# Kernel optimization log

Measured on AMD Instinct MI355X. Metric: run time of the kernel, lower is better.

Reference implementation:

```python
import jax, jax.numpy as jnp
import numpy as np
from jax import lax

# program token ids
PAD, START, END, SCENE, INTERSECT, FILT, RELATE, QUERY = range(8)
SKIP = (PAD, START, END)


def conv2d(x, w, b, dil=1):
    # 'same' padding for odd kernels (3x3 pad=dil, 1x1 pad=0), NCHW/OIHW
    pad = dil * (w.shape[2] // 2)
    y = lax.conv_general_dilated(x, w, (1, 1), [(pad, pad), (pad, pad)],
                                 rhs_dilation=(dil, dil),
                                 dimension_numbers=('NCHW', 'OIHW', 'NCHW'))
    return y + b[None, :, None, None]


def maxpool2(x):
    return lax.reduce_window(x, -jnp.inf, lax.max, (1, 1, 2, 2), (1, 1, 2, 2), 'VALID')


def exec_program(prog, feat_input, p):
    """Run one (concrete) program over a batch of stem features. prog: tuple of ints,
    executed in reversed order exactly like TbDNet.forward."""
    B, _, H, W = feat_input.shape
    output = feat_input
    saved = None
    for t in reversed(prog):
        if t in SKIP:
            continue
        if t == SCENE:
            saved = output
            output = jnp.ones((B, 1, H, W), feat_input.dtype)
        elif t == INTERSECT:  # AndModule: elementwise min of attentions
            output = jnp.minimum(output, saved)
        elif t == FILT:
            a = feat_input * output  # [B,D,H,W] * [B,1,H,W]
            a = jax.nn.relu(conv2d(a, p['att_w1'], p['att_b1']))
            a = jax.nn.relu(conv2d(a, p['att_w2'], p['att_b2']))
            output = jax.nn.sigmoid(conv2d(a, p['att_w3'], p['att_b3']))
        elif t == RELATE:  # RelateModule: dilated conv stack (1,2,4,8,1) -> conv1x1 sigmoid
            a = feat_input * output
            for w, b, d in ((p['rel_w1'], p['rel_b1'], 1), (p['rel_w2'], p['rel_b2'], 2),
                            (p['rel_w3'], p['rel_b3'], 4), (p['rel_w4'], p['rel_b4'], 8),
                            (p['rel_w5'], p['rel_b5'], 1)):
                a = jax.nn.relu(conv2d(a, w, b, d))
            output = jax.nn.sigmoid(conv2d(a, p['rel_w6'], p['rel_b6']))
        elif t == QUERY:
            a = feat_input * output
            a = jax.nn.relu(conv2d(a, p['qry_w1'], p['qry_b1']))
            output = jax.nn.relu(conv2d(a, p['qry_w2'], p['qry_b2']))
    return output


def tbd_forward(feats, programs_np, p):
    B = feats.shape[0]
    stem = jax.nn.relu(conv2d(feats, p['stem_w1'], p['stem_b1']))
    stem = jax.nn.relu(conv2d(stem, p['stem_w2'], p['stem_b2']))  # [B,D,H,W]
    D, H, W = stem.shape[1], stem.shape[2], stem.shape[3]
    # group samples by identical program so dispatch runs batched, not per-sample
    groups = {}
    for n in range(B):
        groups.setdefault(tuple(int(v) for v in programs_np[n]), []).append(n)
    mod_out = jnp.zeros((B, D, H, W), feats.dtype)
    for prog, idxs in groups.items():
        idx = jnp.array(idxs)
        mod_out = mod_out.at[idx].set(exec_program(prog, stem[idx], p))
    # classifier: conv1x1 -> relu -> maxpool2 -> flatten -> fc -> relu -> fc
    x = jax.nn.relu(conv2d(mod_out, p['cls_w'], p['cls_b']))
    x = maxpool2(x)                        # [B,1024,7,7]
    x = x.reshape(B, -1)                   # [B,50176]
    x = jax.nn.relu(x @ p['fc1_w'].T + p['fc1_b'])
    return x @ p['fc2_w'].T + p['fc2_b']   # [B,28]


def setup_inputs() -> dict:
    key = jax.random.key(0)
    ks = iter(jax.random.split(key, 64))
    def rn(shape, s=0.05):
        return jax.random.normal(next(ks), shape, dtype=jnp.float32) * s
    B, Cin, H, W, D, P, L, A = 64, 1024, 14, 14, 128, 1024, 1024, 28
    feats = jax.random.normal(next(ks), (B, Cin, H, W), dtype=jnp.float32)
    # stored programs; execution order is reversed(stored)
    progA = [START, QUERY, FILT, RELATE, FILT, SCENE, END, PAD]            # scene->filter->relate->filter->query
    progB = [START, QUERY, INTERSECT, FILT, SCENE, FILT, SCENE, END]       # two filter branches -> intersect -> query
    programs = jnp.array([progA] * (B // 2) + [progB] * (B // 2), dtype=jnp.int32)
    inp = {'feats': feats, 'programs': programs,
           'stem_w1': rn((D, Cin, 3, 3), 0.02), 'stem_b1': rn((D,)),
           'stem_w2': rn((D, D, 3, 3)), 'stem_b2': rn((D,)),
           'att_w1': rn((D, D, 3, 3)), 'att_b1': rn((D,)),
           'att_w2': rn((D, D, 3, 3)), 'att_b2': rn((D,)),
           'att_w3': rn((1, D, 1, 1)), 'att_b3': rn((1,)),
           'rel_w1': rn((D, D, 3, 3)), 'rel_b1': rn((D,)),
           'rel_w2': rn((D, D, 3, 3)), 'rel_b2': rn((D,)),
           'rel_w3': rn((D, D, 3, 3)), 'rel_b3': rn((D,)),
           'rel_w4': rn((D, D, 3, 3)), 'rel_b4': rn((D,)),
           'rel_w5': rn((D, D, 3, 3)), 'rel_b5': rn((D,)),
           'rel_w6': rn((1, D, 1, 1)), 'rel_b6': rn((1,)),
           'qry_w1': rn((D, D, 3, 3)), 'qry_b1': rn((D,)),
           'qry_w2': rn((D, D, 3, 3)), 'qry_b2': rn((D,)),
           'cls_w': rn((P, D, 1, 1)), 'cls_b': rn((P,)),
           'fc1_w': rn((L, P * (H // 2) * (W // 2)), 0.01), 'fc1_b': rn((L,)),
           'fc2_w': rn((A, L)), 'fc2_b': rn((A,))}
    return inp


PARAM_NAMES = ['stem_w1', 'stem_b1', 'stem_w2', 'stem_b2',
               'att_w1', 'att_b1', 'att_w2', 'att_b2', 'att_w3', 'att_b3',
               'rel_w1', 'rel_b1', 'rel_w2', 'rel_b2', 'rel_w3', 'rel_b3',
               'rel_w4', 'rel_b4', 'rel_w5', 'rel_b5', 'rel_w6', 'rel_b6',
               'qry_w1', 'qry_b1', 'qry_w2', 'qry_b2',
               'cls_w', 'cls_b', 'fc1_w', 'fc1_b', 'fc2_w', 'fc2_b']


def reference(feats, programs, stem_w1, stem_b1, stem_w2, stem_b2,
              att_w1, att_b1, att_w2, att_b2, att_w3, att_b3,
              rel_w1, rel_b1, rel_w2, rel_b2, rel_w3, rel_b3,
              rel_w4, rel_b4, rel_w5, rel_b5, rel_w6, rel_b6,
              qry_w1, qry_b1, qry_w2, qry_b2,
              cls_w, cls_b, fc1_w, fc1_b, fc2_w, fc2_b):
    vals = [stem_w1, stem_b1, stem_w2, stem_b2,
            att_w1, att_b1, att_w2, att_b2, att_w3, att_b3,
            rel_w1, rel_b1, rel_w2, rel_b2, rel_w3, rel_b3,
            rel_w4, rel_b4, rel_w5, rel_b5, rel_w6, rel_b6,
            qry_w1, qry_b1, qry_w2, qry_b2,
            cls_w, cls_b, fc1_w, fc1_b, fc2_w, fc2_b]
    p = dict(zip(PARAM_NAMES, vals))
    return tbd_forward(feats, np.asarray(programs), p)
```

## Files before the change

kernel.cpp:

```cpp
#include <hip/hip_runtime.h>
#include <math.h>


typedef __attribute__((ext_vector_type(8)))  short   short8;
typedef __attribute__((ext_vector_type(8)))  __bf16  bf16x8;
typedef __attribute__((ext_vector_type(4)))  float   f32x4;

#define NROUNDS 15
#define NKS 49

#define B_WSTEM1 0UL
#define B_WSTEM2 2359296UL
#define B_WMOD   2654208UL
#define B_WCLS   5308416UL
#define B_STEM   5570560UL
#define B_XA     8781824UL
#define B_XB     11993088UL
#define B_FEAT   15204352UL
#define B_ATTN   18415616UL
#define B_SAVED  18465792UL
#define B_SCHED  18515968UL
#define B_ACTB   18520064UL
#define B_FC1T   24942592UL
#define B_S1P    B_XB
#define B_FC1P   B_STEM

__device__ __forceinline__ unsigned short f2bf(float f) {
    unsigned int b = __float_as_uint(f);
    b += 0x7fffu + ((b >> 16) & 1u);
    return (unsigned short)(b >> 16);
}
__device__ __forceinline__ float bf2f(unsigned short u) {
    return __uint_as_float(((unsigned int)u) << 16);
}
__device__ __forceinline__ f32x4 mfma16(bf16x8 a, bf16x8 b, f32x4 c) {
    return __builtin_amdgcn_mfma_f32_16x16x32_bf16(a, b, c, 0, 0, 0);
}

struct RepackArgs { const float* src[12]; };

__global__ __launch_bounds__(256) void k_repack(RepackArgs a, char* ws)
{
    const int y = blockIdx.y;
    const float* __restrict__ src = a.src[y];
    int gid = blockIdx.x * 256 + threadIdx.x;
    int gsz = gridDim.x * 256;
    if (y == 11) {
        unsigned short* dst = (unsigned short*)(ws + B_WCLS);
        for (int i = gid; i < 131072; i += gsz) dst[i] = f2bf(src[i]);
    } else {
        const int IC = (y == 0) ? 1024 : 128;
        const int lg = (y == 0) ? 10 : 7;
        unsigned short* dst = (unsigned short*)(ws + ((y == 0) ? B_WSTEM1
                                    : (y == 1) ? B_WSTEM2
                                    : B_WMOD + (size_t)(y - 2) * 294912));
        const int total = 9 << (lg + 7);
        for (int i = gid; i < total; i += gsz) {
            int ic = i & (IC - 1);
            int oc = (i >> lg) & 127;
            int t  = i >> (lg + 7);
            dst[i] = f2bf(src[((size_t)oc * IC + ic) * 9 + t]);
        }
    }
}

__global__ __launch_bounds__(256) void k_decode_init(const int* __restrict__ prog, char* ws)
{
    int gid = blockIdx.x * 256 + threadIdx.x;
    int gsz = gridDim.x * 256;
    float* attn  = (float*)(ws + B_ATTN);
    float* saved = (float*)(ws + B_SAVED);
    for (int i = gid; i < 64 * 196; i += gsz) { attn[i] = 1.0f; saved[i] = 1.0f; }
    unsigned int* fz = (unsigned int*)(ws + B_FEAT);
    for (int i = gid; i < 64 * 25088 / 2; i += gsz) fz[i] = 0u;
    if (gid < 64) {
        int n = gid;
        int ent[NROUNDS];
        for (int r = 0; r < NROUNDS; ++r) ent[r] = 0;
        int rc = 0;
#define ENC(op,wv,dl,g,s,d) ((op)|((wv)<<4)|((dl)<<8)|((g)<<12)|((s)<<13)|((d)<<15))
#define EMIT(v) do { if (rc < NROUNDS) ent[rc++] = (v); } while (0)
        for (int j = 7; j >= 0; --j) {
            int t = prog[n * 8 + j];
            switch (t) {
                case 3: EMIT(ENC(1,0,0,0,0,0)); break;
                case 4: EMIT(ENC(2,0,0,0,0,0)); break;
                case 5:
                    EMIT(ENC(3,0,1,1,3,0));
                    EMIT(ENC(3,1,1,0,0,1));
                    EMIT(ENC(4,0,0,0,1,0));
                    break;
                case 6:
                    EMIT(ENC(3,2,1,1,3,0));
                    EMIT(ENC(3,3,2,0,0,1));
                    EMIT(ENC(3,4,4,0,1,0));
                    EMIT(ENC(3,5,8,0,0,1));
                    EMIT(ENC(3,6,1,0,1,0));
                    EMIT(ENC(4,1,0,0,0,0));
                    break;
                case 7:
                    EMIT(ENC(3,7,1,1,3,0));
                    EMIT(ENC(3,8,1,0,0,2));
                    break;
                default: break;
            }
        }
#undef EMIT
#undef ENC
        int* sched = (int*)(ws + B_SCHED);
        for (int r = 0; r < NROUNDS; ++r) sched[n * NROUNDS + r] = ent[r];
    }
}

__global__ __launch_bounds__(512) void k_stem1p(const float* __restrict__ feats,
                                                const unsigned short* __restrict__ wrep,
                                                char* ws)
{
    __shared__ unsigned short s_img[197 * 136];
    const int bx = blockIdx.x;
    const int n = bx >> 2, ks = bx & 3;
    const int tid = threadIdx.x, lane = tid & 63;
    const int w = tid >> 6, wm = w & 1, wn = w >> 1;
    const int l15 = lane & 15, lq = lane >> 4;

    if (tid < 68) ((unsigned int*)s_img)[196 * 68 + tid] = 0u;

    int pglob[4], pbyt[4], pyv[4], pxv[4];
#pragma unroll
    for (int j = 0; j < 4; ++j) {
        int p  = (wn + 4 * j) * 16 + l15;
        pglob[j] = p;
        int py = p / 14;
        pyv[j] = (p < 196) ? py : 10000;
        pxv[j] = p - py * 14;
        pbyt[j] = p * 272 + lq * 16;
    }
    const int zaddr = 196 * 272 + lq * 16;
    const int nJ = (wn == 0) ? 4 : 3;

    f32x4 acc[4][4];
#pragma unroll
    for (int m = 0; m < 4; ++m)
#pragma unroll
        for (int j = 0; j < 4; ++j) acc[m][j] = (f32x4){0.f, 0.f, 0.f, 0.f};

    const int icg = tid & 31;
    const int qq0 = tid >> 5;

    for (int slab = 0; slab < 2; ++slab) {
        if (slab) __syncthreads();
        const int icb = ks * 256 + slab * 128;
        const float* sf = feats + ((size_t)n * 1024 + icb) * 196;
        for (int qq = qq0; qq < 49; qq += 16) {
            const float* p0 = sf + icg * 4 * 196 + qq * 4;
            float4 r0 = *(const float4*)(p0);
            float4 r1 = *(const float4*)(p0 + 196);
            float4 r2 = *(const float4*)(p0 + 392);
            float4 r3 = *(const float4*)(p0 + 588);
#pragma unroll
            for (int e = 0; e < 4; ++e) {
                uint2 v;
                v.x = (unsigned int)f2bf(((const float*)&r0)[e]) |
                      ((unsigned int)f2bf(((const float*)&r1)[e]) << 16);
                v.y = (unsigned int)f2bf(((const float*)&r2)[e]) |
                      ((unsigned int)f2bf(((const float*)&r3)[e]) << 16);
                *(uint2*)(s_img + (qq * 4 + e) * 136 + icg * 4) = v;
            }
        }
        __syncthreads();

#pragma unroll
        for (int t = 0; t < 9; ++t) {
            const int dy = t / 3 - 1, dx = t % 3 - 1;
            int baddr[4];
#pragma unroll
            for (int j = 0; j < 4; ++j) {
                int yy = pyv[j] + dy, xx = pxv[j] + dx;
                bool ok = ((unsigned)yy < 14u) && ((unsigned)xx < 14u);
                baddr[j] = ok ? (pbyt[j] + (dy * 14 + dx) * 272) : zaddr;
            }
#pragma unroll
            for (int kc = 0; kc < 4; ++kc) {
                const unsigned short* wt = wrep +
                    ((size_t)(t * 128 + wm * 64 + l15) * 1024 + icb + kc * 32 + lq * 8);
                bf16x8 am[4];
#pragma unroll
                for (int m = 0; m < 4; ++m)
                    am[m] = *(const bf16x8*)(wt + (size_t)m * 16 * 1024);
#pragma unroll
                for (int j = 0; j < 4; ++j) {
                    if (j < nJ) {
                        bf16x8 b = *(const bf16x8*)((const char*)s_img + baddr[j] + kc * 64);
#pragma unroll
                        for (int m = 0; m < 4; ++m)
                            acc[m][j] = mfma16(am[m], b, acc[m][j]);
                    }
                }
            }
        }
    }

    unsigned short* part = (unsigned short*)(ws + B_S1P);
#pragma unroll
    for (int m = 0; m < 4; ++m) {
        const int oc = wm * 64 + m * 16 + lq * 4;
#pragma unroll
        for (int j = 0; j < 4; ++j) {
            if (j < nJ) {
                int p = pglob[j];
                if (p < 196) {
                    unsigned int lo = (unsigned int)f2bf(acc[m][j][0]) |
                                      ((unsigned int)f2bf(acc[m][j][1]) << 16);
                    unsigned int hi = (unsigned int)f2bf(acc[m][j][2]) |
                                      ((unsigned int)f2bf(acc[m][j][3]) << 16);
                    uint2 pk; pk.x = lo; pk.y = hi;
                    *(uint2*)(part + (((size_t)ks * 64 + n) * 196 + p) * 128 + oc) = pk;
                }
            }
        }
    }
}

__global__ __launch_bounds__(256) void k_stem1r(const char* __restrict__ ws_c,
                                                const float* __restrict__ bias,
                                                unsigned short* __restrict__ xa)
{
    int i = blockIdx.x * 256 + threadIdx.x;
    const unsigned short* part = (const unsigned short*)(ws_c + B_S1P);
    int oc8 = (i & 15) * 8;
    int np  = i >> 4;
    float s[8] = {};
#pragma unroll
    for (int ks = 0; ks < 4; ++ks) {
        short8 v = *(const short8*)(part + (((size_t)ks * 64) * 196 + np) * 128 + oc8);
#pragma unroll
        for (int e = 0; e < 8; ++e) s[e] += bf2f((unsigned short)v[e]);
    }
    short8 o;
#pragma unroll
    for (int e = 0; e < 8; ++e)
        o[e] = (short)f2bf(fmaxf(s[e] + bias[oc8 + e], 0.f));
    *(short8*)(xa + (size_t)np * 128 + oc8) = o;
}

__device__ void conv_mfma_core(const unsigned short* __restrict__ srcB,
                               const float*  __restrict__ gate,
                               const unsigned short* __restrict__ wrep,
                               const float*  __restrict__ bias,
                               unsigned short* __restrict__ dst,
                               int dil, int oct, int pxh,
                               unsigned short* s_img)
{
    const int tid  = threadIdx.x, lane = tid & 63;
    const int w    = tid >> 6, wm = w & 1, wn = w >> 1;
    const int l15  = lane & 15, lq = lane >> 4;

    if (tid < 68) ((unsigned int*)s_img)[196 * 68 + tid] = 0u;

    int pglob[4], pbyt[4], pyv[4], pxv[4];
#pragma unroll
    for (int j = 0; j < 4; ++j) {
        int nt = wn + 2 * j;
        int p  = (pxh * 7 + nt) * 16 + l15;
        pglob[j] = p;
        int py = p / 14;
        pyv[j] = (p < 196) ? py : 10000;
        pxv[j] = p - py * 14;
        pbyt[j] = p * 272 + lq * 16;
    }
    const int zaddr = 196 * 272 + lq * 16;
    const int nNT = (wn == 0) ? 4 : 3;

    f32x4 acc[4];
#pragma unroll
    for (int j = 0; j < 4; ++j) acc[j] = (f32x4){0.f, 0.f, 0.f, 0.f};

    if (gate) {
        for (int i = tid; i < 196 * 16; i += 256) {
            int p = i >> 4, c8 = (i & 15) * 8;
            short8 v = *(const short8*)(srcB + p * 128 + c8);
            float g = gate[p];
            short8 ov;
#pragma unroll
            for (int e = 0; e < 8; ++e)
                ov[e] = (short)f2bf(bf2f((unsigned short)v[e]) * g);
            *(short8*)(s_img + p * 136 + c8) = ov;
        }
    } else {
        for (int i = tid; i < 196 * 16; i += 256) {
            int p = i >> 4, c8 = (i & 15) * 8;
            *(short8*)(s_img + p * 136 + c8) = *(const short8*)(srcB + p * 128 + c8);
        }
    }
    __syncthreads();

    const unsigned short* wlane = wrep + (size_t)(oct * 32 + wm * 16 + l15) * 128 + lq * 8;
#pragma unroll
    for (int t = 0; t < 9; ++t) {
        const int dy = (t / 3 - 1) * dil, dx = (t % 3 - 1) * dil;
        int baddr[4];
#pragma unroll
        for (int j = 0; j < 4; ++j) {
            int yy = pyv[j] + dy, xx = pxv[j] + dx;
            bool ok = ((unsigned)yy < 14u) && ((unsigned)xx < 14u);
            baddr[j] = ok ? (pbyt[j] + (dy * 14 + dx) * 272) : zaddr;
        }
        const unsigned short* wt = wlane + (size_t)(t * 128) * 128;
#pragma unroll
        for (int kc = 0; kc < 4; ++kc) {
            bf16x8 a0 = *(const bf16x8*)(wt + kc * 32);
#pragma unroll
            for (int j = 0; j < 4; ++j) {
                if (j < nNT) {
                    bf16x8 b = *(const bf16x8*)((const char*)s_img + baddr[j] + kc * 64);
                    acc[j] = mfma16(a0, b, acc[j]);
                }
            }
        }
    }

    const int oc = oct * 32 + wm * 16 + lq * 4;
    const float4 b4 = *(const float4*)(bias + oc);
#pragma unroll
    for (int j = 0; j < 4; ++j) {
        if (j < nNT) {
            int p = pglob[j];
            if (p < 196) {
                float v0 = fmaxf(acc[j][0] + b4.x, 0.f);
                float v1 = fmaxf(acc[j][1] + b4.y, 0.f);
                float v2 = fmaxf(acc[j][2] + b4.z, 0.f);
                float v3 = fmaxf(acc[j][3] + b4.w, 0.f);
                uint2 pk;
                pk.x = (unsigned int)f2bf(v0) | ((unsigned int)f2bf(v1) << 16);
                pk.y = (unsigned int)f2bf(v2) | ((unsigned int)f2bf(v3) << 16);
                *(uint2*)(dst + p * 128 + oc) = pk;
            }
        }
    }
}

__global__ __launch_bounds__(256) void k_conv_stem2(const unsigned short* __restrict__ srcBall,
                                                    const unsigned short* __restrict__ wrep,
                                                    const float* __restrict__ bias,
                                                    unsigned short* __restrict__ dstall)
{
    __shared__ unsigned short s_img[197 * 136];
    const int n = blockIdx.x >> 3, oct = (blockIdx.x >> 1) & 3, pxh = blockIdx.x & 1;
    conv_mfma_core(srcBall + (size_t)n * 25088, nullptr, wrep, bias,
                   dstall + (size_t)n * 25088, 1, oct, pxh, s_img);
}

struct RArgs {
    char* ws;
    const float* mbias[9];
    const float* w1x1[2];
    const float* b1x1[2];
};

__global__ __launch_bounds__(256) void k_round(RArgs a, int r)
{
    __shared__ unsigned short s_img[197 * 136];
    const int bx = blockIdx.x;
    const int n = bx >> 3, oct = (bx >> 1) & 3, pxh = bx & 1;
    char* ws = a.ws;
    const int* sched = (const int*)(ws + B_SCHED);
    const int e = sched[n * NROUNDS + r];
    const int op = e & 15;
    if (op == 0) return;
    float* attn  = (float*)(ws + B_ATTN)  + n * 196;
    float* saved = (float*)(ws + B_SAVED) + n * 196;
    if (op == 1 || op == 2) {
        if ((bx & 7) == 0 && threadIdx.x < 196) {
            int p = threadIdx.x;
            if (op == 1) { saved[p] = attn[p]; attn[p] = 1.0f; }
            else         attn[p] = fminf(attn[p], saved[p]);
        }
        return;
    }
    const int wset = (e >> 4) & 15, dil = (e >> 8) & 15, gatef = (e >> 12) & 1;
    const int srcid = (e >> 13) & 3, dstid = (e >> 15) & 3;
    const unsigned short* src = (const unsigned short*)(ws +
            (srcid == 3 ? B_STEM : srcid == 1 ? B_XB : B_XA)) + (size_t)n * 25088;
    if (op == 4) {
        if ((bx & 7) == 0 && threadIdx.x < 196) {
            int p = threadIdx.x;
            const float* wv = a.w1x1[wset];
            float acc = a.b1x1[wset][0];
            const unsigned short* row = src + p * 128;
#pragma unroll 8
            for (int ic = 0; ic < 128; ++ic) acc += bf2f(row[ic]) * wv[ic];
            attn[p] = 1.0f / (1.0f + __expf(-acc));
        }
        return;
    }
    unsigned short* dst = (unsigned short*)(ws +
            (dstid == 2 ? B_FEAT : dstid == 1 ? B_XB : B_XA)) + (size_t)n * 25088;
    const unsigned short* wrep = (const unsigned short*)(ws + B_WMOD) + (size_t)wset * 9 * 128 * 128;
    conv_mfma_core(src, gatef ? attn : nullptr, wrep, a.mbias[wset], dst,
                   dil, oct, pxh, s_img);
}

__global__ __launch_bounds__(256) void k_cls_pool(const unsigned short* __restrict__ featall,
                                                  const unsigned short* __restrict__ clsw,
                                                  const float* __restrict__ clsb,
                                                  unsigned short* __restrict__ actB)
{
    __shared__ char smem[197 * 272 + 64 * 200 * 4];
    unsigned short* s_img = (unsigned short*)smem;
    float* s_pool = (float*)(smem + 197 * 272);
    const int n = blockIdx.x >> 4, pt = blockIdx.x & 15;
    const int tid = threadIdx.x, lane = tid & 63, w = tid >> 6;
    const int l15 = lane & 15, lq = lane >> 4;
    const unsigned short* feat = featall + (size_t)n * 25088;

    if (tid < 68) ((unsigned int*)s_img)[196 * 68 + tid] = 0u;
    for (int i = tid; i < 196 * 16; i += 256) {
        int p = i >> 4, c8 = (i & 15) * 8;
        *(short8*)(s_img + p * 136 + c8) = *(const short8*)(feat + p * 128 + c8);
    }
    f32x4 acc[14];
#pragma unroll
    for (int j = 0; j < 14; ++j) acc[j] = (f32x4){0.f, 0.f, 0.f, 0.f};
    __syncthreads();

    const unsigned short* wl = clsw + (size_t)(pt * 64 + w * 16 + l15) * 128 + lq * 8;
#pragma unroll
    for (int kc = 0; kc < 4; ++kc) {
        bf16x8 a0 = *(const bf16x8*)(wl + kc * 32);
#pragma unroll
        for (int j = 0; j < 14; ++j) {
            int p = j * 16 + l15;
            int ba = (p < 196) ? (p * 272 + lq * 16 + kc * 64) : (196 * 272 + lq * 16);
            bf16x8 b = *(const bf16x8*)((const char*)s_img + ba);
            acc[j] = mfma16(a0, b, acc[j]);
        }
    }
    const int oc = pt * 64 + w * 16 + lq * 4;
    const float4 b4 = *(const float4*)(clsb + oc);
    const int pl = w * 16 + lq * 4;
#pragma unroll
    for (int j = 0; j < 14; ++j) {
        int p = j * 16 + l15;
        if (p < 196) {
            s_pool[(pl + 0) * 200 + p] = fmaxf(acc[j][0] + b4.x, 0.f);
            s_pool[(pl + 1) * 200 + p] = fmaxf(acc[j][1] + b4.y, 0.f);
            s_pool[(pl + 2) * 200 + p] = fmaxf(acc[j][2] + b4.z, 0.f);
            s_pool[(pl + 3) * 200 + p] = fmaxf(acc[j][3] + b4.w, 0.f);
        }
    }
    __syncthreads();
    for (int i = tid; i < 64 * 49; i += 256) {
        int plx = i / 49, q = i - plx * 49;
        int py = q / 7, qx = q - py * 7;
        const float* rp = s_pool + plx * 200 + py * 28 + qx * 2;
        float m = fmaxf(fmaxf(rp[0], rp[1]), fmaxf(rp[14], rp[15]));
        int k = (pt * 64 + plx) * 49 + q;
        int kb = k >> 6, lq2 = (k >> 4) & 3, hi = (k >> 3) & 1, e = k & 7;
        actB[((((size_t)kb * 4 + lq2) * 2 + hi) * 64 + n) * 8 + e] = f2bf(m);
    }
}

__global__ __launch_bounds__(256) void k_fc1p(const unsigned short* __restrict__ actB,
                                              const float* __restrict__ w,
                                              float* __restrict__ part)
{
    __shared__ unsigned short s_w[64 * 264];
    const int jt = blockIdx.x & 15, ks = blockIdx.x >> 4;
    const int tid = threadIdx.x, lane = tid & 63, wv = tid >> 6;
    const int l15 = lane & 15, lq = lane >> 4;
    const int k0 = ks * 1024;
    const int r4 = tid & 3, l4 = (tid >> 2) & 15, rw = tid >> 6;

    f32x4 acc[4];
#pragma unroll
    for (int t = 0; t < 4; ++t) acc[t] = (f32x4){0.f, 0.f, 0.f, 0.f};

    float4 pf[4][4];

#define FC1_LOAD(ss_) do {                                                        \
    _Pragma("unroll")                                                             \
    for (int pass = 0; pass < 4; ++pass) {                                        \
        const int row_ = pass * 16 + rw * 4 + r4;                                 \
        const float* wp_ = w + (size_t)(jt * 64 + row_) * 50176 + k0              \
                             + (ss_) * 256 + l4 * 16;                             \
        pf[pass][0] = *(const float4*)(wp_);                                      \
        pf[pass][1] = *(const float4*)(wp_ + 4);                                  \
        pf[pass][2] = *(const float4*)(wp_ + 8);                                  \
        pf[pass][3] = *(const float4*)(wp_ + 12);                                 \
    } } while (0)

    FC1_LOAD(0);

    for (int ss = 0; ss < 4; ++ss) {
        __syncthreads();
#pragma unroll
        for (int pass = 0; pass < 4; ++pass) {
            const int row = pass * 16 + rw * 4 + r4;
            bf16x8 c0, c1;
            c0[0] = (__bf16)pf[pass][0].x; c0[1] = (__bf16)pf[pass][0].y;
            c0[2] = (__bf16)pf[pass][0].z; c0[3] = (__bf16)pf[pass][0].w;
            c0[4] = (__bf16)pf[pass][1].x; c0[5] = (__bf16)pf[pass][1].y;
            c0[6] = (__bf16)pf[pass][1].z; c0[7] = (__bf16)pf[pass][1].w;
            c1[0] = (__bf16)pf[pass][2].x; c1[1] = (__bf16)pf[pass][2].y;
            c1[2] = (__bf16)pf[pass][2].z; c1[3] = (__bf16)pf[pass][2].w;
            c1[4] = (__bf16)pf[pass][3].x; c1[5] = (__bf16)pf[pass][3].y;
            c1[6] = (__bf16)pf[pass][3].z; c1[7] = (__bf16)pf[pass][3].w;
            *(bf16x8*)(s_w + row * 264 + l4 * 16)     = c0;
            *(bf16x8*)(s_w + row * 264 + l4 * 16 + 8) = c1;
        }
        __syncthreads();
        if (ss < 3) FC1_LOAD(ss + 1);

        const unsigned short* arow = s_w + (wv * 16 + l15) * 264;
#pragma unroll
        for (int kk = 0; kk < 8; ++kk) {
            bf16x8 a = *(const bf16x8*)(arow + kk * 32 + lq * 8);
            const int kglob = k0 + ss * 256 + kk * 32 + lq * 8;
            const int kb = kglob >> 6, lq2 = (kglob >> 4) & 3, hi = (kglob >> 3) & 1;
            const unsigned short* bp = actB +
                ((((size_t)kb * 4 + lq2) * 2 + hi) * 64 + l15) * 8;
#pragma unroll
            for (int t = 0; t < 4; ++t) {
                bf16x8 b = *(const bf16x8*)(bp + t * 128);
                acc[t] = mfma16(a, b, acc[t]);
            }
        }
    }
#undef FC1_LOAD

    float* pbase = part + ((size_t)ks * 1024 + jt * 64 + wv * 16 + lq * 4) * 64 + l15;
#pragma unroll
    for (int t = 0; t < 4; ++t)
#pragma unroll
        for (int r = 0; r < 4; ++r)
            pbase[(size_t)r * 64 + t * 16] = acc[t][r];
}

__global__ __launch_bounds__(256) void k_fc1r(const float* __restrict__ part,
                                              const float* __restrict__ b,
                                              float* __restrict__ fc1T)
{
    int i = blockIdx.x * 256 + threadIdx.x;
    if (i >= 65536) return;
    float s = 0.0f;
    for (int ks = 0; ks < NKS; ++ks) s += part[(size_t)ks * 65536 + i];
    int j = i >> 6;
    fc1T[i] = fmaxf(s + b[j], 0.0f);
}

__global__ __launch_bounds__(256) void k_fc2(const float* __restrict__ fc1T,
                                             const float* __restrict__ w,
                                             const float* __restrict__ b,
                                             float* __restrict__ out)
{
    __shared__ float red[256];
    const int a_ = blockIdx.x;
    const int tid = threadIdx.x, lane = tid & 63, q = tid >> 6;
    float acc = 0.0f;
    const float* wr = w + (size_t)a_ * 1024;
    for (int k = q * 256; k < q * 256 + 256; ++k)
        acc = fmaf(fc1T[k * 64 + lane], wr[k], acc);
    red[tid] = acc;
    __syncthreads();
    if (q == 0) {
        float s = red[tid] + red[tid + 64] + red[tid + 128] + red[tid + 192] + b[a_];
        out[lane * 28 + a_] = s;
    }
}

extern "C" void kernel_launch(void* const* d_in, const int* in_sizes, int n_in,
                              void* d_out, int out_size, void* d_ws, size_t ws_size,
                              hipStream_t stream)
{
    const float* feats = (const float*)d_in[0];
    const int*   prog  = (const int*)d_in[1];
    char* ws  = (char*)d_ws;
    float* out = (float*)d_out;

    RepackArgs ra;
    ra.src[0]  = (const float*)d_in[2];
    ra.src[1]  = (const float*)d_in[4];
    ra.src[2]  = (const float*)d_in[6];
    ra.src[3]  = (const float*)d_in[8];
    ra.src[4]  = (const float*)d_in[12];
    ra.src[5]  = (const float*)d_in[14];
    ra.src[6]  = (const float*)d_in[16];
    ra.src[7]  = (const float*)d_in[18];
    ra.src[8]  = (const float*)d_in[20];
    ra.src[9]  = (const float*)d_in[24];
    ra.src[10] = (const float*)d_in[26];
    ra.src[11] = (const float*)d_in[28];

    k_repack<<<dim3(64, 12), 256, 0, stream>>>(ra, ws);

    k_stem1p<<<256, 512, 0, stream>>>(feats, (const unsigned short*)(ws + B_WSTEM1), ws);
    k_stem1r<<<784, 256, 0, stream>>>(ws, (const float*)d_in[3],
                                      (unsigned short*)(ws + B_XA));

    k_decode_init<<<256, 256, 0, stream>>>(prog, ws);

    k_conv_stem2<<<512, 256, 0, stream>>>((const unsigned short*)(ws + B_XA),
                                          (const unsigned short*)(ws + B_WSTEM2),
                                          (const float*)d_in[5],
                                          (unsigned short*)(ws + B_STEM));

    RArgs ga;
    ga.ws = ws;
    ga.mbias[0] = (const float*)d_in[7];
    ga.mbias[1] = (const float*)d_in[9];
    ga.mbias[2] = (const float*)d_in[13];
    ga.mbias[3] = (const float*)d_in[15];
    ga.mbias[4] = (const float*)d_in[17];
    ga.mbias[5] = (const float*)d_in[19];
    ga.mbias[6] = (const float*)d_in[21];
    ga.mbias[7] = (const float*)d_in[25];
    ga.mbias[8] = (const float*)d_in[27];
    ga.w1x1[0]  = (const float*)d_in[10];
    ga.w1x1[1]  = (const float*)d_in[22];
    ga.b1x1[0]  = (const float*)d_in[11];
    ga.b1x1[1]  = (const float*)d_in[23];

    for (int r = 0; r < NROUNDS; ++r)
        k_round<<<512, 256, 0, stream>>>(ga, r);

    k_cls_pool<<<1024, 256, 0, stream>>>((const unsigned short*)(ws + B_FEAT),
                                         (const unsigned short*)(ws + B_WCLS),
                                         (const float*)d_in[29],
                                         (unsigned short*)(ws + B_ACTB));
    k_fc1p<<<784, 256, 0, stream>>>((const unsigned short*)(ws + B_ACTB),
                                    (const float*)d_in[30], (float*)(ws + B_FC1P));
    k_fc1r<<<256, 256, 0, stream>>>((const float*)(ws + B_FC1P), (const float*)d_in[31],
                                    (float*)(ws + B_FC1T));
    k_fc2<<<28, 256, 0, stream>>>((const float*)(ws + B_FC1T), (const float*)d_in[32],
                                  (const float*)d_in[33], out);
}
```

Baseline: 546.1 us.

## Fuse scene/intersect/1x1 heads into conv rounds and split stem/fc1 reductions finer

Removes the separate scene, intersect and 1x1-sigmoid rounds by folding them into the conv epilogue and the next conv's gate prologue. The 1x1 projection is now accumulated with atomics into per-slot buffers, and the sigmoid plus scene/intersect bookkeeping is applied when the next gated conv starts. This cuts the round count from 15 to 12 launches. Separately, the stem1 and fc1 K-splits are doubled to raise parallelism, which moves partial buffers to new workspace offsets and adds more partial-sum reduction work plus atomic contention.

```diff
diff --git a/kernel.cpp b/kernel.cpp
--- a/kernel.cpp
+++ b/kernel.cpp
@@ -6,8 +6,8 @@
 typedef __attribute__((ext_vector_type(8)))  __bf16  bf16x8;
 typedef __attribute__((ext_vector_type(4)))  float   f32x4;
 
-#define NROUNDS 15
-#define NKS 49
+#define NROUNDS 12
+#define NKS 98
 
 #define B_WSTEM1 0UL
 #define B_WSTEM2 2359296UL
@@ -22,8 +22,9 @@
 #define B_SCHED  18515968UL
 #define B_ACTB   18520064UL
 #define B_FC1T   24942592UL
-#define B_S1P    B_XB
-#define B_FC1P   B_STEM
+#define B_P1X1   25204736UL
+#define B_S1P    67108864UL
+#define B_FC1P   100663296UL
 
 __device__ __forceinline__ unsigned short f2bf(float f) {
     unsigned int b = __float_as_uint(f);
@@ -70,43 +71,57 @@
     int gsz = gridDim.x * 256;
     float* attn  = (float*)(ws + B_ATTN);
     float* saved = (float*)(ws + B_SAVED);
+    float* p1    = (float*)(ws + B_P1X1);
     for (int i = gid; i < 64 * 196; i += gsz) { attn[i] = 1.0f; saved[i] = 1.0f; }
+    for (int i = gid; i < 8 * 64 * 196; i += gsz) p1[i] = 0.0f;
     unsigned int* fz = (unsigned int*)(ws + B_FEAT);
     for (int i = gid; i < 64 * 25088 / 2; i += gsz) fz[i] = 0u;
     if (gid < 64) {
         int n = gid;
         int ent[NROUNDS];
         for (int r = 0; r < NROUNDS; ++r) ent[r] = 0;
-        int rc = 0;
-#define ENC(op,wv,dl,g,s,d) ((op)|((wv)<<4)|((dl)<<8)|((g)<<12)|((s)<<13)|((d)<<15))
+        int rc = 0, nslot = 0;
+        int pscene = 0, pinter = 0, pmat = 0, pmw = 0;
+#define PREBITS ((pscene<<17)|(pinter<<18)|(pmat<<19)|(pmw<<22))
+#define CLRPRE  (pscene = pinter = pmat = pmw = 0)
 #define EMIT(v) do { if (rc < NROUNDS) ent[rc++] = (v); } while (0)
         for (int j = 7; j >= 0; --j) {
             int t = prog[n * 8 + j];
             switch (t) {
-                case 3: EMIT(ENC(1,0,0,0,0,0)); break;
-                case 4: EMIT(ENC(2,0,0,0,0,0)); break;
-                case 5:
-                    EMIT(ENC(3,0,1,1,3,0));
-                    EMIT(ENC(3,1,1,0,0,1));
-                    EMIT(ENC(4,0,0,0,1,0));
+                case 3: pscene = 1; break;
+                case 4: pinter = 1; break;
+                case 5: {
+                    int e1 = 3 | (0<<4) | (1<<8) | (1<<12) | (2<<13) | (0<<15) | PREBITS;
+                    CLRPRE; EMIT(e1);
+                    int e2 = 3 | (1<<4) | (1<<8) | (0<<12) | (0<<13) | (1<<15)
+                               | (1<<23) | (0<<24) | (nslot<<25);
+                    EMIT(e2);
+                    pmat = nslot + 1; pmw = 0; nslot++;
                     break;
-                case 6:
-                    EMIT(ENC(3,2,1,1,3,0));
-                    EMIT(ENC(3,3,2,0,0,1));
-                    EMIT(ENC(3,4,4,0,1,0));
-                    EMIT(ENC(3,5,8,0,0,1));
-                    EMIT(ENC(3,6,1,0,1,0));
-                    EMIT(ENC(4,1,0,0,0,0));
+                }
+                case 6: {
+                    int e1 = 3 | (2<<4) | (1<<8) | (1<<12) | (2<<13) | (0<<15) | PREBITS;
+                    CLRPRE; EMIT(e1);
+                    EMIT(3 | (3<<4) | (2<<8) | (0<<12) | (0<<13) | (1<<15));
+                    EMIT(3 | (4<<4) | (4<<8) | (0<<12) | (1<<13) | (0<<15));
+                    EMIT(3 | (5<<4) | (8<<8) | (0<<12) | (0<<13) | (1<<15));
+                    EMIT(3 | (6<<4) | (1<<8) | (0<<12) | (1<<13) | (0<<15)
+                           | (1<<23) | (1<<24) | (nslot<<25));
+                    pmat = nslot + 1; pmw = 1; nslot++;
                     break;
-                case 7:
-                    EMIT(ENC(3,7,1,1,3,0));
-                    EMIT(ENC(3,8,1,0,0,2));
+                }
+                case 7: {
+                    int e1 = 3 | (7<<4) | (1<<8) | (1<<12) | (2<<13) | (0<<15) | PREBITS;
+                    CLRPRE; EMIT(e1);
+                    EMIT(3 | (8<<4) | (1<<8) | (0<<12) | (0<<13) | (2<<15));
                     break;
+                }
                 default: break;
             }
         }
 #undef EMIT
-#undef ENC
+#undef PREBITS
+#undef CLRPRE
         int* sched = (int*)(ws + B_SCHED);
         for (int r = 0; r < NROUNDS; ++r) sched[n * NROUNDS + r] = ent[r];
     }
@@ -118,7 +133,7 @@
 {
     __shared__ unsigned short s_img[197 * 136];
     const int bx = blockIdx.x;
-    const int n = bx >> 2, ks = bx & 3;
+    const int n = bx >> 3, ks = bx & 7;
     const int tid = threadIdx.x, lane = tid & 63;
     const int w = tid >> 6, wm = w & 1, wn = w >> 1;
     const int l15 = lane & 15, lq = lane >> 4;
@@ -146,55 +161,52 @@
 
     const int icg = tid & 31;
     const int qq0 = tid >> 5;
-
-    for (int slab = 0; slab < 2; ++slab) {
-        if (slab) __syncthreads();
-        const int icb = ks * 256 + slab * 128;
-        const float* sf = feats + ((size_t)n * 1024 + icb) * 196;
-        for (int qq = qq0; qq < 49; qq += 16) {
-            const float* p0 = sf + icg * 4 * 196 + qq * 4;
-            float4 r0 = *(const float4*)(p0);
-            float4 r1 = *(const float4*)(p0 + 196);
-            float4 r2 = *(const float4*)(p0 + 392);
-            float4 r3 = *(const float4*)(p0 + 588);
-#pragma unroll
-            for (int e = 0; e < 4; ++e) {
-                uint2 v;
-                v.x = (unsigned int)f2bf(((const float*)&r0)[e]) |
-                      ((unsigned int)f2bf(((const float*)&r1)[e]) << 16);
-                v.y = (unsigned int)f2bf(((const float*)&r2)[e]) |
-                      ((unsigned int)f2bf(((const float*)&r3)[e]) << 16);
-                *(uint2*)(s_img + (qq * 4 + e) * 136 + icg * 4) = v;
-            }
-        }
-        __syncthreads();
-
-#pragma unroll
-        for (int t = 0; t < 9; ++t) {
-            const int dy = t / 3 - 1, dx = t % 3 - 1;
-            int baddr[4];
+    const int icb = ks * 128;
+
+    const float* sf = feats + ((size_t)n * 1024 + icb) * 196;
+    for (int qq = qq0; qq < 49; qq += 16) {
+        const float* p0 = sf + icg * 4 * 196 + qq * 4;
+        float4 r0 = *(const float4*)(p0);
+        float4 r1 = *(const float4*)(p0 + 196);
+        float4 r2 = *(const float4*)(p0 + 392);
+        float4 r3 = *(const float4*)(p0 + 588);
+#pragma unroll
+        for (int e = 0; e < 4; ++e) {
+            uint2 v;
+            v.x = (unsigned int)f2bf(((const float*)&r0)[e]) |
+                  ((unsigned int)f2bf(((const float*)&r1)[e]) << 16);
+            v.y = (unsigned int)f2bf(((const float*)&r2)[e]) |
+                  ((unsigned int)f2bf(((const float*)&r3)[e]) << 16);
+            *(uint2*)(s_img + (qq * 4 + e) * 136 + icg * 4) = v;
+        }
+    }
+    __syncthreads();
+
+#pragma unroll
+    for (int t = 0; t < 9; ++t) {
+        const int dy = t / 3 - 1, dx = t % 3 - 1;
+        int baddr[4];
+#pragma unroll
+        for (int j = 0; j < 4; ++j) {
+            int yy = pyv[j] + dy, xx = pxv[j] + dx;
+            bool ok = ((unsigned)yy < 14u) && ((unsigned)xx < 14u);
+            baddr[j] = ok ? (pbyt[j] + (dy * 14 + dx) * 272) : zaddr;
+        }
+#pragma unroll
+        for (int kc = 0; kc < 4; ++kc) {
+            const unsigned short* wt = wrep +
+                ((size_t)(t * 128 + wm * 64 + l15) * 1024 + icb + kc * 32 + lq * 8);
+            bf16x8 am[4];
+#pragma unroll
+            for (int m = 0; m < 4; ++m)
+                am[m] = *(const bf16x8*)(wt + (size_t)m * 16 * 1024);
 #pragma unroll
             for (int j = 0; j < 4; ++j) {
-                int yy = pyv[j] + dy, xx = pxv[j] + dx;
-                bool ok = ((unsigned)yy < 14u) && ((unsigned)xx < 14u);
-                baddr[j] = ok ? (pbyt[j] + (dy * 14 + dx) * 272) : zaddr;
-            }
-#pragma unroll
-            for (int kc = 0; kc < 4; ++kc) {
-                const unsigned short* wt = wrep +
-                    ((size_t)(t * 128 + wm * 64 + l15) * 1024 + icb + kc * 32 + lq * 8);
-                bf16x8 am[4];
-#pragma unroll
-                for (int m = 0; m < 4; ++m)
-                    am[m] = *(const bf16x8*)(wt + (size_t)m * 16 * 1024);
-#pragma unroll
-                for (int j = 0; j < 4; ++j) {
-                    if (j < nJ) {
-                        bf16x8 b = *(const bf16x8*)((const char*)s_img + baddr[j] + kc * 64);
-#pragma unroll
-                        for (int m = 0; m < 4; ++m)
-                            acc[m][j] = mfma16(am[m], b, acc[m][j]);
-                    }
+                if (j < nJ) {
+                    bf16x8 b = *(const bf16x8*)((const char*)s_img + baddr[j] + kc * 64);
+#pragma unroll
+                    for (int m = 0; m < 4; ++m)
+                        acc[m][j] = mfma16(am[m], b, acc[m][j]);
                 }
             }
         }
@@ -231,7 +243,7 @@
     int np  = i >> 4;
     float s[8] = {};
 #pragma unroll
-    for (int ks = 0; ks < 4; ++ks) {
+    for (int ks = 0; ks < 8; ++ks) {
         short8 v = *(const short8*)(part + (((size_t)ks * 64) * 196 + np) * 128 + oc8);
 #pragma unroll
         for (int e = 0; e < 8; ++e) s[e] += bf2f((unsigned short)v[e]);
@@ -243,13 +255,15 @@
     *(short8*)(xa + (size_t)np * 128 + oc8) = o;
 }
 
-__device__ void conv_mfma_core(const unsigned short* __restrict__ srcB,
-                               const float*  __restrict__ gate,
-                               const unsigned short* __restrict__ wrep,
-                               const float*  __restrict__ bias,
-                               unsigned short* __restrict__ dst,
-                               int dil, int oct, int pxh,
-                               unsigned short* s_img)
+__device__ void conv_core32(const unsigned short* __restrict__ srcB,
+                            const float* __restrict__ s_gate,
+                            const unsigned short* __restrict__ wrep,
+                            const float* __restrict__ bias,
+                            unsigned short* __restrict__ dst,
+                            int dil, int oct, int pxh,
+                            unsigned short* s_img,
+                            int post, const float* __restrict__ pwv,
+                            float* __restrict__ pdst)
 {
     const int tid  = threadIdx.x, lane = tid & 63;
     const int w    = tid >> 6, wm = w & 1, wn = w >> 1;
@@ -275,11 +289,11 @@
 #pragma unroll
     for (int j = 0; j < 4; ++j) acc[j] = (f32x4){0.f, 0.f, 0.f, 0.f};
 
-    if (gate) {
+    if (s_gate) {
         for (int i = tid; i < 196 * 16; i += 256) {
             int p = i >> 4, c8 = (i & 15) * 8;
             short8 v = *(const short8*)(srcB + p * 128 + c8);
-            float g = gate[p];
+            float g = s_gate[p];
             short8 ov;
 #pragma unroll
             for (int e = 0; e < 8; ++e)
@@ -321,6 +335,8 @@
 
     const int oc = oct * 32 + wm * 16 + lq * 4;
     const float4 b4 = *(const float4*)(bias + oc);
+    float4 wv4;
+    if (post) wv4 = *(const float4*)(pwv + oc);
 #pragma unroll
     for (int j = 0; j < 4; ++j) {
         if (j < nNT) {
@@ -334,6 +350,10 @@
                 pk.x = (unsigned int)f2bf(v0) | ((unsigned int)f2bf(v1) << 16);
                 pk.y = (unsigned int)f2bf(v2) | ((unsigned int)f2bf(v3) << 16);
                 *(uint2*)(dst + p * 128 + oc) = pk;
+                if (post) {
+                    float s = v0 * wv4.x + v1 * wv4.y + v2 * wv4.z + v3 * wv4.w;
+                    atomicAdd(pdst + p, s);
+                }
             }
         }
     }
@@ -346,8 +366,8 @@
 {
     __shared__ unsigned short s_img[197 * 136];
     const int n = blockIdx.x >> 3, oct = (blockIdx.x >> 1) & 3, pxh = blockIdx.x & 1;
-    conv_mfma_core(srcBall + (size_t)n * 25088, nullptr, wrep, bias,
-                   dstall + (size_t)n * 25088, 1, oct, pxh, s_img);
+    conv_core32(srcBall + (size_t)n * 25088, nullptr, wrep, bias,
+                dstall + (size_t)n * 25088, 1, oct, pxh, s_img, 0, nullptr, nullptr);
 }
 
 struct RArgs {
@@ -360,44 +380,49 @@
 __global__ __launch_bounds__(256) void k_round(RArgs a, int r)
 {
     __shared__ unsigned short s_img[197 * 136];
+    __shared__ float s_gate[196];
     const int bx = blockIdx.x;
     const int n = bx >> 3, oct = (bx >> 1) & 3, pxh = bx & 1;
     char* ws = a.ws;
     const int* sched = (const int*)(ws + B_SCHED);
     const int e = sched[n * NROUNDS + r];
-    const int op = e & 15;
-    if (op == 0) return;
+    if ((e & 15) == 0) return;
+    const int tid = threadIdx.x;
+    const int wset = (e >> 4) & 15, dil = (e >> 8) & 15, gatef = (e >> 12) & 1;
+    const int srcid = (e >> 13) & 3, dstid = (e >> 15) & 3;
+    const int fscene = (e >> 17) & 1, finter = (e >> 18) & 1;
+    const int mslot = (e >> 19) & 7, mw = (e >> 22) & 1;
+    const int post = (e >> 23) & 1, pw = (e >> 24) & 1, pslot = (e >> 25) & 7;
+
     float* attn  = (float*)(ws + B_ATTN)  + n * 196;
     float* saved = (float*)(ws + B_SAVED) + n * 196;
-    if (op == 1 || op == 2) {
-        if ((bx & 7) == 0 && threadIdx.x < 196) {
-            int p = threadIdx.x;
-            if (op == 1) { saved[p] = attn[p]; attn[p] = 1.0f; }
-            else         attn[p] = fminf(attn[p], saved[p]);
-        }
-        return;
-    }
-    const int wset = (e >> 4) & 15, dil = (e >> 8) & 15, gatef = (e >> 12) & 1;
-    const int srcid = (e >> 13) & 3, dstid = (e >> 15) & 3;
+    float* p1    = (float*)(ws + B_P1X1);
+
+    if (gatef) {
+        if (tid < 196) {
+            float cur = attn[tid];
+            if (mslot) {
+                float pv = p1[(size_t)(mslot - 1) * 12544 + n * 196 + tid];
+                cur = 1.0f / (1.0f + __expf(-(pv + a.b1x1[mw][0])));
+            }
+            if (fscene) { saved[tid] = cur; cur = 1.0f; }
+            if (finter) { cur = fminf(cur, saved[tid]); }
+            if (mslot | fscene | finter) attn[tid] = cur;
+            s_gate[tid] = cur;
+        }
+        __syncthreads();
+    }
+
     const unsigned short* src = (const unsigned short*)(ws +
-            (srcid == 3 ? B_STEM : srcid == 1 ? B_XB : B_XA)) + (size_t)n * 25088;
-    if (op == 4) {
-        if ((bx & 7) == 0 && threadIdx.x < 196) {
-            int p = threadIdx.x;
-            const float* wv = a.w1x1[wset];
-            float acc = a.b1x1[wset][0];
-            const unsigned short* row = src + p * 128;
-#pragma unroll 8
-            for (int ic = 0; ic < 128; ++ic) acc += bf2f(row[ic]) * wv[ic];
-            attn[p] = 1.0f / (1.0f + __expf(-acc));
-        }
-        return;
-    }
+            (srcid == 2 ? B_STEM : srcid == 1 ? B_XB : B_XA)) + (size_t)n * 25088;
     unsigned short* dst = (unsigned short*)(ws +
             (dstid == 2 ? B_FEAT : dstid == 1 ? B_XB : B_XA)) + (size_t)n * 25088;
     const unsigned short* wrep = (const unsigned short*)(ws + B_WMOD) + (size_t)wset * 9 * 128 * 128;
-    conv_mfma_core(src, gatef ? attn : nullptr, wrep, a.mbias[wset], dst,
-                   dil, oct, pxh, s_img);
+
+    conv_core32(src, gatef ? s_gate : nullptr, wrep, a.mbias[wset], dst,
+                dil, oct, pxh, s_img,
+                post, post ? a.w1x1[pw] : nullptr,
+                post ? (p1 + (size_t)pslot * 12544 + n * 196) : nullptr);
 }
 
 __global__ __launch_bounds__(256) void k_cls_pool(const unsigned short* __restrict__ featall,
@@ -468,7 +493,7 @@
     const int jt = blockIdx.x & 15, ks = blockIdx.x >> 4;
     const int tid = threadIdx.x, lane = tid & 63, wv = tid >> 6;
     const int l15 = lane & 15, lq = lane >> 4;
-    const int k0 = ks * 1024;
+    const int k0 = ks * 512;
     const int r4 = tid & 3, l4 = (tid >> 2) & 15, rw = tid >> 6;
 
     f32x4 acc[4];
@@ -491,7 +516,7 @@
 
     FC1_LOAD(0);
 
-    for (int ss = 0; ss < 4; ++ss) {
+    for (int ss = 0; ss < 2; ++ss) {
         __syncthreads();
 #pragma unroll
         for (int pass = 0; pass < 4; ++pass) {
@@ -509,7 +534,7 @@
             *(bf16x8*)(s_w + row * 264 + l4 * 16 + 8) = c1;
         }
         __syncthreads();
-        if (ss < 3) FC1_LOAD(ss + 1);
+        if (ss < 1) FC1_LOAD(1);
 
         const unsigned short* arow = s_w + (wv * 16 + l15) * 264;
 #pragma unroll
@@ -592,12 +617,11 @@
     ra.src[11] = (const float*)d_in[28];
 
     k_repack<<<dim3(64, 12), 256, 0, stream>>>(ra, ws);
-
-    k_stem1p<<<256, 512, 0, stream>>>(feats, (const unsigned short*)(ws + B_WSTEM1), ws);
+    k_decode_init<<<256, 256, 0, stream>>>(prog, ws);
+
+    k_stem1p<<<512, 512, 0, stream>>>(feats, (const unsigned short*)(ws + B_WSTEM1), ws);
     k_stem1r<<<784, 256, 0, stream>>>(ws, (const float*)d_in[3],
                                       (unsigned short*)(ws + B_XA));
-
-    k_decode_init<<<256, 256, 0, stream>>>(prog, ws);
 
     k_conv_stem2<<<512, 256, 0, stream>>>((const unsigned short*)(ws + B_XA),
                                           (const unsigned short*)(ws + B_WSTEM2),
@@ -627,8 +651,8 @@
                                          (const unsigned short*)(ws + B_WCLS),
                                          (const float*)d_in[29],
                                          (unsigned short*)(ws + B_ACTB));
-    k_fc1p<<<784, 256, 0, stream>>>((const unsigned short*)(ws + B_ACTB),
-                                    (const float*)d_in[30], (float*)(ws + B_FC1P));
+    k_fc1p<<<1568, 256, 0, stream>>>((const unsigned short*)(ws + B_ACTB),
+                                     (const float*)d_in[30], (float*)(ws + B_FC1P));
     k_fc1r<<<256, 256, 0, stream>>>((const float*)(ws + B_FC1P), (const float*)d_in[31],
                                     (float*)(ws + B_FC1T));
     k_fc2<<<28, 256, 0, stream>>>((const float*)(ws + B_FC1T), (const float*)d_in[32],
```

Result: faster. 525.9 us (-3.7%).
